# Performance work log

Measured on AMD Instinct MI355X. Metric: run time of the kernel, lower is better.

## Reference

```python
import jax, jax.numpy as jnp
import numpy as np

L, D, H, KV, HD, KVL, I, PL = 8, 2048, 8, 2, 256, 4096, 8192, 256
FULL = (4,)          # layers with full (global) attention / global RoPE
POS = 2047           # current decode position (cache write slot)
N_REP = H // KV      # GQA expansion factor


def rms(x, eps=1e-6):
    # RMSNorm without scale (v_norm); scale applied by caller where needed
    return x * jax.lax.rsqrt(jnp.mean(x * x, axis=-1, keepdims=True) + eps)


def rope(x, cos, sin):
    half = HD // 2
    rot = jnp.concatenate([-x[..., half:], x[..., :half]], axis=-1)
    return x * cos + rot * sin


def _rope_tables(theta):
    inv = 1.0 / (theta ** (np.arange(0, HD, 2, dtype=np.float32) / HD))
    ang = jnp.asarray(POS * inv, dtype=jnp.float32)
    return jnp.concatenate([jnp.cos(ang)] * 2), jnp.concatenate([jnp.sin(ang)] * 2)


def setup_inputs() -> dict:
    key = jax.random.key(0)
    ks = jax.random.split(key, 24)
    r = lambda k, s, sc=0.02: jax.random.normal(k, s, jnp.float32) * sc
    gains = lambda k, s: 1.0 + jax.random.normal(k, s, jnp.float32) * 0.02
    cos_s, sin_s = _rope_tables(10000.0)
    cos_f, sin_f = _rope_tables(1000000.0)
    um = jnp.zeros((1, 1, KVL, 1), jnp.float32).at[0, 0, POS, 0].set(1.0)
    mask = jnp.where(jnp.arange(KVL) <= POS, 0.0, -1e9).astype(jnp.float32)
    return {
        "hidden_states": r(ks[0], (1, 1, D), 1.0),
        "causal_mask": mask,
        "update_mask": um,
        "per_layer_combined": r(ks[1], (1, 1, L * PL), 1.0),
        "cos_s": cos_s, "sin_s": sin_s, "cos_f": cos_f, "sin_f": sin_f,
        "K_in": r(ks[2], (L, KV, KVL, HD)),
        "V_in": r(ks[3], (L, KV, KVL, HD)),
        "w_q": r(ks[4], (L, H * HD, D)),
        "w_k": r(ks[5], (L, KV * HD, D)),
        "w_v": r(ks[6], (L, KV * HD, D)),
        "w_o": r(ks[7], (L, D, H * HD)),
        "g_in_ln": gains(ks[8], (L, D)),
        "g_q_norm": gains(ks[9], (L, HD)),
        "g_k_norm": gains(ks[10], (L, HD)),
        "g_post_attn_ln": gains(ks[11], (L, D)),
        "g_pre_ff_ln": gains(ks[12], (L, D)),
        "g_post_ff_ln": gains(ks[13], (L, D)),
        "w_gate": r(ks[14], (L, I, D)),
        "w_up": r(ks[15], (L, I, D)),
        "w_down": r(ks[16], (L, D, I)),
        "w_plg": r(ks[17], (L, PL, D)),
        "w_plp": r(ks[18], (L, D, PL)),
        "g_post_pl_ln": gains(ks[19], (L, D)),
        "layer_scalar": jnp.ones((L,), jnp.float32),
    }


def reference(hidden_states, causal_mask, update_mask, per_layer_combined,
              cos_s, sin_s, cos_f, sin_f, K_in, V_in,
              w_q, w_k, w_v, w_o,
              g_in_ln, g_q_norm, g_k_norm, g_post_attn_ln, g_pre_ff_ln, g_post_ff_ln,
              w_gate, w_up, w_down, w_plg, w_plp, g_post_pl_ln, layer_scalar):
    um = update_mask[0, 0]          # [KVL,1] one-hot at write position
    h = hidden_states[0, 0]         # [D], batch=1/seq=1 decode
    K_outs, V_outs = [], []
    for i in range(L):
        cos, sin = (cos_f, sin_f) if i in FULL else (cos_s, sin_s)
        # --- attention block ---
        res = h
        x = rms(h) * g_in_ln[i]
        q = rms((w_q[i] @ x).reshape(H, HD)) * g_q_norm[i]
        q = rope(q, cos, sin)                                   # [H,HD]
        k = rms((w_k[i] @ x).reshape(KV, HD)) * g_k_norm[i]
        k = rope(k, cos, sin)                                   # [KV,HD]
        v = rms((w_v[i] @ x).reshape(KV, HD))                    # v_norm (no scale)
        # full-tensor masked blend = KV cache write (faithful to source)
        Ko = K_in[i] * (1.0 - um) + k[:, None, :] * um          # [KV,KVL,HD]
        Vo = V_in[i] * (1.0 - um) + v[:, None, :] * um
        K_outs.append(Ko); V_outs.append(Vo)
        Ke = jnp.repeat(Ko, N_REP, axis=0)                      # GQA expand [H,KVL,HD]
        Ve = jnp.repeat(Vo, N_REP, axis=0)
        scores = jnp.einsum('hd,hkd->hk', q, Ke) + causal_mask  # no 1/sqrt(hd) in source
        attn = jax.nn.softmax(scores, axis=-1)
        ao = jnp.einsum('hk,hkd->hd', attn, Ve).reshape(H * HD)
        ao = rms(w_o[i] @ ao) * g_post_attn_ln[i]
        h = res + ao
        # --- gated MLP ---
        res = h
        xm = rms(h) * g_pre_ff_ln[i]
        m = w_down[i] @ (jax.nn.gelu(w_gate[i] @ xm, approximate=True) * (w_up[i] @ xm))
        h = res + rms(m) * g_post_ff_ln[i]
        # --- per-layer input gating ---
        res = h
        pls = per_layer_combined[0, 0, i * PL:(i + 1) * PL]     # [PL]
        g = jax.nn.gelu(w_plg[i] @ h, approximate=True) * pls
        h = res + rms(w_plp[i] @ g) * g_post_pl_ln[i]
        h = h * layer_scalar[i]
    return (h[None, None, :], jnp.stack(K_outs), jnp.stack(V_outs))
```

## Files before the change

kernel.cpp:

```cpp
#include <hip/hip_runtime.h>

#define NL   8
#define DIM  2048
#define NH   8
#define NKV  2
#define HD   256
#define KVL  4096
#define FFI  8192
#define PLD  256
#define POS  2047
#define NCH  128
#define CP   16

__device__ __forceinline__ float dot4(float4 a, float4 b){
  return a.x*b.x + a.y*b.y + a.z*b.z + a.w*b.w;
}

__device__ __forceinline__ float waveAllSum(float v){
#pragma unroll
  for(int o=1;o<64;o<<=1) v += __shfl_xor(v,o,64);
  return v;
}

__device__ __forceinline__ float blockSum256(float v, float* red){
  int lane = threadIdx.x & 63, w = threadIdx.x >> 6;
  v = waveAllSum(v);
  __syncthreads();
  if(lane==0) red[w] = v;
  __syncthreads();
  return red[0]+red[1]+red[2]+red[3];
}

__device__ __forceinline__ float gelu_tanh(float v){
  return 0.5f*v*(1.0f + tanhf(0.7978845608028654f*(v + 0.044715f*v*v*v)));
}

__device__ __forceinline__ float4 normRope(const float* __restrict__ raw, int lane,
    const float* __restrict__ gain, const float* __restrict__ cosT,
    const float* __restrict__ sinT, bool doRope){
  float4 v4 = ((const float4*)raw)[lane];
  float ss = waveAllSum(dot4(v4,v4));
  float sc = rsqrtf(ss*(1.f/HD) + 1e-6f);
  float4 n;
  if(gain){
    float4 g4 = ((const float4*)gain)[lane];
    n.x=v4.x*sc*g4.x; n.y=v4.y*sc*g4.y; n.z=v4.z*sc*g4.z; n.w=v4.w*sc*g4.w;
  } else {
    n.x=v4.x*sc; n.y=v4.y*sc; n.z=v4.z*sc; n.w=v4.w*sc;
  }
  if(!doRope) return n;
  float4 np;
  np.x=__shfl_xor(n.x,32,64); np.y=__shfl_xor(n.y,32,64);
  np.z=__shfl_xor(n.z,32,64); np.w=__shfl_xor(n.w,32,64);
  float4 c4 = ((const float4*)cosT)[lane];
  float4 s4 = ((const float4*)sinT)[lane];
  float sg = (lane < 32) ? -1.f : 1.f;
  float4 o;
  o.x = n.x*c4.x + sg*np.x*s4.x;
  o.y = n.y*c4.y + sg*np.y*s4.y;
  o.z = n.z*c4.z + sg*np.z*s4.z;
  o.w = n.w*c4.w + sg*np.w*s4.w;
  return o;
}

__global__ __launch_bounds__(256) void qkv_k(
    const float* __restrict__ Wq, const float* __restrict__ Wk,
    const float* __restrict__ Wv,
    const float* __restrict__ hC, const float* __restrict__ u,
    const float* __restrict__ g_pl, const float* __restrict__ lsc,
    const float* __restrict__ g_in, const float* __restrict__ hidden,
    float* __restrict__ hA, float* __restrict__ qkv){
  __shared__ float xs[DIM];
  __shared__ float red[4];
  int tid = threadIdx.x;
  float hv[8];
  if(hidden){
#pragma unroll
    for(int i=0;i<8;i++) hv[i] = hidden[tid + i*256];
  } else {
    float uv[8]; float ss1 = 0.f;
#pragma unroll
    for(int i=0;i<8;i++){ uv[i] = u[tid + i*256]; ss1 += uv[i]*uv[i]; }
    ss1 = blockSum256(ss1, red);
    float r1 = rsqrtf(ss1*(1.f/DIM) + 1e-6f);
    float ls = lsc[0];
#pragma unroll
    for(int i=0;i<8;i++){
      int idx = tid + i*256;
      hv[i] = (hC[idx] + uv[i]*r1*g_pl[idx])*ls;
    }
  }
  float ss2 = 0.f;
#pragma unroll
  for(int i=0;i<8;i++) ss2 += hv[i]*hv[i];
  ss2 = blockSum256(ss2, red);
  float r2 = rsqrtf(ss2*(1.f/DIM) + 1e-6f);
#pragma unroll
  for(int i=0;i<8;i++){
    int idx = tid + i*256;
    xs[idx] = hv[i]*r2*g_in[idx];
    if(blockIdx.x==0) hA[idx] = hv[i];
  }
  __syncthreads();
  int lane = tid & 63, wv = tid >> 6;
  int r = blockIdx.x*4 + wv;
  const float* W; int row;
  if(r < 2048){ W = Wq; row = r; }
  else if(r < 2560){ W = Wk; row = r - 2048; }
  else { W = Wv; row = r - 2560; }
  const float4* Wr = (const float4*)(W + (size_t)row*DIM);
  const float4* xs4 = (const float4*)xs;
  float4 w8[8];
#pragma unroll
  for(int i=0;i<8;i++) w8[i] = Wr[i*64+lane];
  float acc = 0.f;
#pragma unroll
  for(int i=0;i<8;i++) acc += dot4(w8[i], xs4[i*64+lane]);
  acc = waveAllSum(acc);
  if(lane==0) qkv[r] = acc;
}

__global__ __launch_bounds__(256) void attn_k(
    const float* __restrict__ qkvb,
    const float* __restrict__ gq, const float* __restrict__ gk,
    const float* __restrict__ cosT, const float* __restrict__ sinT,
    float* __restrict__ Kl, float* __restrict__ Vl,
    float* __restrict__ pm, float* __restrict__ pl, float* __restrict__ po){
  int b = blockIdx.x, tid = threadIdx.x, lane = tid & 63, wv = tid >> 6;

  if(b == NKV*NCH){
    int kvv = wv >> 1, isV = wv & 1;
    const float* raw = qkvb + (isV ? 2560 : 2048) + kvv*HD;
    float4 o = normRope(raw, lane, isV ? nullptr : gk, cosT, sinT, !isV);
    float* dst = (isV ? Vl : Kl) + ((size_t)kvv*KVL + POS)*HD;
    ((float4*)dst)[lane] = o;
    return;
  }

  int kv = b & 1, c = b >> 1;
  __shared__ float q_s[4][HD];
  __shared__ float vf_s[HD];
  __shared__ float s_s[4][CP];
  __shared__ float s_w[4][CP];
  bool fresh = (c == NCH-1);

  {
    float4 o = normRope(qkvb + (kv*4 + wv)*HD, lane, gq, cosT, sinT, true);
    ((float4*)q_s[wv])[lane] = o;
  }
  float4 kf4 = {0,0,0,0};
  if(fresh){
    if(wv == 3) kf4 = normRope(qkvb + 2048 + kv*HD, lane, gk, cosT, sinT, true);
    if(wv == 1){
      float4 o = normRope(qkvb + 2560 + kv*HD, lane, nullptr, cosT, sinT, false);
      ((float4*)vf_s)[lane] = o;
    }
  }
  __syncthreads();

  float4 q4[4];
#pragma unroll
  for(int hh=0;hh<4;hh++) q4[hh] = ((const float4*)q_s[hh])[lane];
  const float4* Kp = (const float4*)(Kl + ((size_t)kv*KVL + c*CP)*HD);
#pragma unroll
  for(int j=0;j<4;j++){
    int p = wv*4 + j;
    float4 k4 = (fresh && p==CP-1) ? kf4 : Kp[(size_t)p*64 + lane];
    float d0 = dot4(k4,q4[0]), d1 = dot4(k4,q4[1]);
    float d2 = dot4(k4,q4[2]), d3 = dot4(k4,q4[3]);
    d0 = waveAllSum(d0); d1 = waveAllSum(d1);
    d2 = waveAllSum(d2); d3 = waveAllSum(d3);
    if(lane==0){ s_s[0][p]=d0; s_s[1][p]=d1; s_s[2][p]=d2; s_s[3][p]=d3; }
  }
  __syncthreads();

  if(tid < 64){
    int hh = tid >> 4, pp = tid & 15;
    float s = s_s[hh][pp];
    float m = s;
#pragma unroll
    for(int o=1;o<16;o<<=1) m = fmaxf(m, __shfl_xor(m,o,64));
    float e = __expf(s - m);
    float ls = e;
#pragma unroll
    for(int o=1;o<16;o<<=1) ls += __shfl_xor(ls,o,64);
    s_w[hh][pp] = e;
    if(pp==0){ int hg = kv*4 + hh; pm[hg*NCH + c] = m; pl[hg*NCH + c] = ls; }
  }
  __syncthreads();

  int d = tid;
  const float* Vp = Vl + ((size_t)kv*KVL + c*CP)*HD;
  float vv[CP];
#pragma unroll
  for(int p2=0;p2<CP;p2++) vv[p2] = Vp[(size_t)p2*HD + d];
  if(fresh) vv[CP-1] = vf_s[d];
  float acc[4] = {0.f,0.f,0.f,0.f};
#pragma unroll
  for(int p2=0;p2<CP;p2++){
#pragma unroll
    for(int hh=0;hh<4;hh++) acc[hh] += s_w[hh][p2]*vv[p2];
  }
#pragma unroll
  for(int hh=0;hh<4;hh++)
    po[((size_t)(kv*4+hh)*NCH + c)*HD + d] = acc[hh];
}

__global__ __launch_bounds__(256) void attn_c(const float* __restrict__ pm,
    const float* __restrict__ pl, const float* __restrict__ po, float* __restrict__ ao){
  int h = blockIdx.x, tid = threadIdx.x;
  __shared__ float sm[NCH], sl[NCH], se[NCH];
  if(tid < NCH){ sm[tid] = pm[h*NCH+tid]; sl[tid] = pl[h*NCH+tid]; }
  __syncthreads();
  float M = -1e30f;
  for(int c=0;c<NCH;c++) M = fmaxf(M, sm[c]);
  if(tid < NCH) se[tid] = __expf(sm[tid]-M);
  __syncthreads();
  float Lh = 0.f;
  for(int c=0;c<NCH;c++) Lh += sl[c]*se[c];
  float a0=0.f, a1=0.f, a2=0.f, a3=0.f;
#pragma unroll 1
  for(int c=0;c<NCH;c+=4){
    a0 += po[((size_t)h*NCH + c  )*HD + tid]*se[c];
    a1 += po[((size_t)h*NCH + c+1)*HD + tid]*se[c+1];
    a2 += po[((size_t)h*NCH + c+2)*HD + tid]*se[c+2];
    a3 += po[((size_t)h*NCH + c+3)*HD + tid]*se[c+3];
  }
  ao[h*HD + tid] = (a0+a1+a2+a3) / Lh;
}

template<int C>
__global__ __launch_bounds__(256) void gemv_k(const float* __restrict__ W,
    const float* __restrict__ x, float* __restrict__ y){
  __shared__ float xs[C];
  for(int i=threadIdx.x; i<C/4; i+=256)
    ((float4*)xs)[i] = ((const float4*)x)[i];
  __syncthreads();
  int lane = threadIdx.x & 63, wv = threadIdx.x >> 6;
  int r = blockIdx.x*4 + wv;
  const float4* Wr = (const float4*)(W + (size_t)r*C);
  const float4* xs4 = (const float4*)xs;
  float acc = 0.f;
#pragma unroll
  for(int ii=0;ii<C/2048;ii++){
    float4 w8[8];
#pragma unroll
    for(int i=0;i<8 && ii*8+i < C/256;i++) w8[i] = Wr[(ii*8+i)*64+lane];
#pragma unroll
    for(int i=0;i<8 && ii*8+i < C/256;i++) acc += dot4(w8[i], xs4[(ii*8+i)*64+lane]);
  }
  if(C < 2048){
    float4 w1 = Wr[lane];
    acc = dot4(w1, xs4[lane]);
  }
  acc = waveAllSum(acc);
  if(lane==0) y[r] = acc;
}

__global__ __launch_bounds__(256) void gateup_k(const float* __restrict__ Wg,
    const float* __restrict__ Wu, const float* __restrict__ y,
    const float* __restrict__ hA, const float* __restrict__ g_pa,
    const float* __restrict__ g_pf, float* __restrict__ hB, float* __restrict__ t){
  __shared__ float xs[DIM];
  __shared__ float red[4];
  int tid = threadIdx.x;
  float yv[8]; float ss1 = 0.f;
#pragma unroll
  for(int i=0;i<8;i++){ yv[i] = y[tid + i*256]; ss1 += yv[i]*yv[i]; }
  ss1 = blockSum256(ss1, red);
  float r1 = rsqrtf(ss1*(1.f/DIM) + 1e-6f);
  float hv[8]; float ss2 = 0.f;
#pragma unroll
  for(int i=0;i<8;i++){
    int idx = tid + i*256;
    hv[i] = hA[idx] + yv[i]*r1*g_pa[idx];
    ss2 += hv[i]*hv[i];
  }
  ss2 = blockSum256(ss2, red);
  float r2 = rsqrtf(ss2*(1.f/DIM) + 1e-6f);
#pragma unroll
  for(int i=0;i<8;i++){
    int idx = tid + i*256;
    xs[idx] = hv[i]*r2*g_pf[idx];
    if(blockIdx.x==0) hB[idx] = hv[i];
  }
  __syncthreads();
  int lane = tid & 63, wv = tid >> 6;
  int j = blockIdx.x*4 + wv;
  const float4* Gr = (const float4*)(Wg + (size_t)j*DIM);
  const float4* Ur = (const float4*)(Wu + (size_t)j*DIM);
  const float4* xs4 = (const float4*)xs;
  float4 g8[8], u8[8];
#pragma unroll
  for(int i=0;i<8;i++) g8[i] = Gr[i*64+lane];
#pragma unroll
  for(int i=0;i<8;i++) u8[i] = Ur[i*64+lane];
  float ag = 0.f, au = 0.f;
#pragma unroll
  for(int i=0;i<8;i++){
    float4 bv = xs4[i*64+lane];
    ag += dot4(g8[i], bv);
    au += dot4(u8[i], bv);
  }
  ag = waveAllSum(ag);
  au = waveAllSum(au);
  if(lane==0) t[j] = gelu_tanh(ag)*au;
}

__global__ __launch_bounds__(256) void down_k(const float* __restrict__ Wd,
    const float* __restrict__ t, float* __restrict__ mv){
  __shared__ float red[4];
  int tid = threadIdx.x, lane = tid & 63, wv = tid >> 6;
  int r = blockIdx.x;
  const float4* Wr = (const float4*)(Wd + (size_t)r*FFI) + wv*512;
  const float4* tp = (const float4*)t + wv*512;
  float4 w8[8], t8[8];
#pragma unroll
  for(int i=0;i<8;i++) w8[i] = Wr[i*64+lane];
#pragma unroll
  for(int i=0;i<8;i++) t8[i] = tp[i*64+lane];
  float acc = 0.f;
#pragma unroll
  for(int i=0;i<8;i++) acc += dot4(w8[i], t8[i]);
  acc = waveAllSum(acc);
  if(lane==0) red[wv] = acc;
  __syncthreads();
  if(tid==0) mv[r] = red[0]+red[1]+red[2]+red[3];
}

__global__ __launch_bounds__(256) void plg_k(const float* __restrict__ W,
    const float* __restrict__ mv, const float* __restrict__ hB,
    const float* __restrict__ g_ff, const float* __restrict__ pls,
    float* __restrict__ hCout, float* __restrict__ gb){
  __shared__ float xs[DIM];
  __shared__ float red[4];
  int tid = threadIdx.x;
  float mvv[8]; float ss1 = 0.f;
#pragma unroll
  for(int i=0;i<8;i++){ mvv[i] = mv[tid + i*256]; ss1 += mvv[i]*mvv[i]; }
  ss1 = blockSum256(ss1, red);
  float r1 = rsqrtf(ss1*(1.f/DIM) + 1e-6f);
#pragma unroll
  for(int i=0;i<8;i++){
    int idx = tid + i*256;
    float hc = hB[idx] + mvv[i]*r1*g_ff[idx];
    xs[idx] = hc;
    if(blockIdx.x==0) hCout[idx] = hc;
  }
  __syncthreads();
  int lane = tid & 63, wv = tid >> 6;
  int r = blockIdx.x*4 + wv;
  const float4* Wr = (const float4*)(W + (size_t)r*DIM);
  const float4* xs4 = (const float4*)xs;
  float4 w8[8];
#pragma unroll
  for(int i=0;i<8;i++) w8[i] = Wr[i*64+lane];
  float acc = 0.f;
#pragma unroll
  for(int i=0;i<8;i++) acc += dot4(w8[i], xs4[i*64+lane]);
  acc = waveAllSum(acc);
  if(lane==0) gb[r] = gelu_tanh(acc)*pls[r];
}

__global__ __launch_bounds__(256) void final_k(const float* __restrict__ u,
    const float* __restrict__ hC, const float* __restrict__ g_pl,
    const float* __restrict__ lsc, float* __restrict__ out){
  __shared__ float red[4];
  int tid = threadIdx.x;
  float uv[8]; float ss1 = 0.f;
#pragma unroll
  for(int i=0;i<8;i++){ uv[i] = u[tid + i*256]; ss1 += uv[i]*uv[i]; }
  ss1 = blockSum256(ss1, red);
  float r1 = rsqrtf(ss1*(1.f/DIM) + 1e-6f);
  float ls = lsc[0];
#pragma unroll
  for(int i=0;i<8;i++){
    int idx = tid + i*256;
    out[idx] = (hC[idx] + uv[i]*r1*g_pl[idx])*ls;
  }
}

extern "C" void kernel_launch(void* const* d_in, const int* in_sizes, int n_in,
                              void* d_out, int out_size, void* d_ws, size_t ws_size,
                              hipStream_t stream){
  const float* hidden   = (const float*)d_in[0];
  const float* plc      = (const float*)d_in[3];
  const float* cos_s    = (const float*)d_in[4];
  const float* sin_s    = (const float*)d_in[5];
  const float* cos_f    = (const float*)d_in[6];
  const float* sin_f    = (const float*)d_in[7];
  const float* K_in     = (const float*)d_in[8];
  const float* V_in     = (const float*)d_in[9];
  const float* w_q      = (const float*)d_in[10];
  const float* w_k      = (const float*)d_in[11];
  const float* w_v      = (const float*)d_in[12];
  const float* w_o      = (const float*)d_in[13];
  const float* g_in_ln  = (const float*)d_in[14];
  const float* g_q_norm = (const float*)d_in[15];
  const float* g_k_norm = (const float*)d_in[16];
  const float* g_pa_ln  = (const float*)d_in[17];
  const float* g_pf_ln  = (const float*)d_in[18];
  const float* g_ff_ln  = (const float*)d_in[19];
  const float* w_gate   = (const float*)d_in[20];
  const float* w_up     = (const float*)d_in[21];
  const float* w_down   = (const float*)d_in[22];
  const float* w_plg    = (const float*)d_in[23];
  const float* w_plp    = (const float*)d_in[24];
  const float* g_pl_ln  = (const float*)d_in[25];
  const float* l_scal   = (const float*)d_in[26];

  float* out  = (float*)d_out;
  float* outK = out + DIM;
  float* outV = outK + (size_t)NL*NKV*KVL*HD;

  float* ws   = (float*)d_ws;
  float* hA   = ws;
  float* hB   = ws + 2048;
  float* hC   = ws + 4096;
  float* qkvb = ws + 6144;
  float* y    = ws + 9216;
  float* t    = ws + 11264;
  float* mv   = ws + 19456;
  float* gb   = ws + 21504;
  float* u    = ws + 21760;
  float* pm   = ws + 23808;
  float* pl   = ws + 24832;
  float* po   = ws + 25856;
  float* ao   = ws + 288000;

  (void)hipMemcpyAsync(outK, K_in, (size_t)NL*NKV*KVL*HD*sizeof(float),
                       hipMemcpyDeviceToDevice, stream);
  (void)hipMemcpyAsync(outV, V_in, (size_t)NL*NKV*KVL*HD*sizeof(float),
                       hipMemcpyDeviceToDevice, stream);

  for(int l=0;l<NL;l++){
    const float* cosT = (l==4) ? cos_f : cos_s;
    const float* sinT = (l==4) ? sin_f : sin_s;
    float* Kl = outK + (size_t)l*NKV*KVL*HD;
    float* Vl = outV + (size_t)l*NKV*KVL*HD;

    qkv_k<<<768,256,0,stream>>>(
        w_q + (size_t)l*NH*HD*DIM, w_k + (size_t)l*NKV*HD*DIM,
        w_v + (size_t)l*NKV*HD*DIM,
        hC, u,
        (l>0) ? g_pl_ln + (size_t)(l-1)*DIM : g_pl_ln,
        (l>0) ? l_scal + (l-1) : l_scal,
        g_in_ln + (size_t)l*DIM,
        (l==0) ? hidden : nullptr,
        hA, qkvb);

    attn_k<<<NKV*NCH+1,256,0,stream>>>(qkvb, g_q_norm + l*HD, g_k_norm + l*HD,
                                       cosT, sinT, Kl, Vl, pm, pl, po);

    attn_c<<<NH,256,0,stream>>>(pm, pl, po, ao);

    gemv_k<DIM><<<512,256,0,stream>>>(w_o + (size_t)l*DIM*NH*HD, ao, y);

    gateup_k<<<FFI/4,256,0,stream>>>(w_gate + (size_t)l*FFI*DIM,
                                     w_up + (size_t)l*FFI*DIM,
                                     y, hA, g_pa_ln + (size_t)l*DIM,
                                     g_pf_ln + (size_t)l*DIM, hB, t);

    down_k<<<DIM,256,0,stream>>>(w_down + (size_t)l*DIM*FFI, t, mv);

    plg_k<<<PLD/4,256,0,stream>>>(w_plg + (size_t)l*PLD*DIM, mv, hB,
                                  g_ff_ln + (size_t)l*DIM, plc + l*PLD, hC, gb);

    gemv_k<PLD><<<512,256,0,stream>>>(w_plp + (size_t)l*DIM*PLD, gb, u);
  }

  final_k<<<1,256,0,stream>>>(u, hC, g_pl_ln + (size_t)(NL-1)*DIM,
                              l_scal + (NL-1), out);
}
```

Before: 809.2 us.

## Fuse per-layer kernels: attn-combine+Wo, gate/up+down with atomics, plg+plp

Cuts each layer from seven launches to four. The attention combine is folded into the Wo GEMV, gate/up and down projections become one kernel that accumulates down-proj partials with atomicAdd, and the per-layer gate and projection are merged into one kernel in which every block recomputes the full plg GEMV redundantly. Attention now reads K/V from the input buffers instead of the copied output, which removes the dependency on the memcpy. Chunk count is halved and chunk size doubled. The aim is to cut launch overhead and intermediate round-trips, at the cost of atomic contention, lower parallelism in several kernels, and redundant plg work.

```diff
diff --git a/kernel.cpp b/kernel.cpp
--- a/kernel.cpp
+++ b/kernel.cpp
@@ -9,8 +9,8 @@
 #define FFI  8192
 #define PLD  256
 #define POS  2047
-#define NCH  128
-#define CP   16
+#define NCH  64
+#define CP   32
 
 __device__ __forceinline__ float dot4(float4 a, float4 b){
   return a.x*b.x + a.y*b.y + a.z*b.z + a.w*b.w;
@@ -66,10 +66,10 @@
 __global__ __launch_bounds__(256) void qkv_k(
     const float* __restrict__ Wq, const float* __restrict__ Wk,
     const float* __restrict__ Wv,
-    const float* __restrict__ hC, const float* __restrict__ u,
+    const float* __restrict__ hFF, const float* __restrict__ u,
     const float* __restrict__ g_pl, const float* __restrict__ lsc,
     const float* __restrict__ g_in, const float* __restrict__ hidden,
-    float* __restrict__ hA, float* __restrict__ qkv){
+    float* __restrict__ hRes, float* __restrict__ qkv){
   __shared__ float xs[DIM];
   __shared__ float red[4];
   int tid = threadIdx.x;
@@ -87,7 +87,7 @@
 #pragma unroll
     for(int i=0;i<8;i++){
       int idx = tid + i*256;
-      hv[i] = (hC[idx] + uv[i]*r1*g_pl[idx])*ls;
+      hv[i] = (hFF[idx] + uv[i]*r1*g_pl[idx])*ls;
     }
   }
   float ss2 = 0.f;
@@ -99,7 +99,7 @@
   for(int i=0;i<8;i++){
     int idx = tid + i*256;
     xs[idx] = hv[i]*r2*g_in[idx];
-    if(blockIdx.x==0) hA[idx] = hv[i];
+    if(blockIdx.x==0) hRes[idx] = hv[i];
   }
   __syncthreads();
   int lane = tid & 63, wv = tid >> 6;
@@ -124,6 +124,7 @@
     const float* __restrict__ qkvb,
     const float* __restrict__ gq, const float* __restrict__ gk,
     const float* __restrict__ cosT, const float* __restrict__ sinT,
+    const float* __restrict__ Ki, const float* __restrict__ Vi,
     float* __restrict__ Kl, float* __restrict__ Vl,
     float* __restrict__ pm, float* __restrict__ pl, float* __restrict__ po){
   int b = blockIdx.x, tid = threadIdx.x, lane = tid & 63, wv = tid >> 6;
@@ -144,10 +145,8 @@
   __shared__ float s_w[4][CP];
   bool fresh = (c == NCH-1);
 
-  {
-    float4 o = normRope(qkvb + (kv*4 + wv)*HD, lane, gq, cosT, sinT, true);
-    ((float4*)q_s[wv])[lane] = o;
-  }
+  { float4 o = normRope(qkvb + (kv*4 + wv)*HD, lane, gq, cosT, sinT, true);
+    ((float4*)q_s[wv])[lane] = o; }
   float4 kf4 = {0,0,0,0};
   if(fresh){
     if(wv == 3) kf4 = normRope(qkvb + 2048 + kv*HD, lane, gk, cosT, sinT, true);
@@ -161,10 +160,10 @@
   float4 q4[4];
 #pragma unroll
   for(int hh=0;hh<4;hh++) q4[hh] = ((const float4*)q_s[hh])[lane];
-  const float4* Kp = (const float4*)(Kl + ((size_t)kv*KVL + c*CP)*HD);
-#pragma unroll
-  for(int j=0;j<4;j++){
-    int p = wv*4 + j;
+  const float4* Kp = (const float4*)(Ki + ((size_t)kv*KVL + c*CP)*HD);
+#pragma unroll
+  for(int j=0;j<8;j++){
+    int p = wv*8 + j;
     float4 k4 = (fresh && p==CP-1) ? kf4 : Kp[(size_t)p*64 + lane];
     float d0 = dot4(k4,q4[0]), d1 = dot4(k4,q4[1]);
     float d2 = dot4(k4,q4[2]), d3 = dot4(k4,q4[3]);
@@ -174,96 +173,95 @@
   }
   __syncthreads();
 
-  if(tid < 64){
-    int hh = tid >> 4, pp = tid & 15;
+  if(tid < 128){
+    int hh = tid >> 5, pp = tid & 31;
     float s = s_s[hh][pp];
     float m = s;
 #pragma unroll
-    for(int o=1;o<16;o<<=1) m = fmaxf(m, __shfl_xor(m,o,64));
+    for(int o=1;o<32;o<<=1) m = fmaxf(m, __shfl_xor(m,o,64));
     float e = __expf(s - m);
     float ls = e;
 #pragma unroll
-    for(int o=1;o<16;o<<=1) ls += __shfl_xor(ls,o,64);
+    for(int o=1;o<32;o<<=1) ls += __shfl_xor(ls,o,64);
     s_w[hh][pp] = e;
     if(pp==0){ int hg = kv*4 + hh; pm[hg*NCH + c] = m; pl[hg*NCH + c] = ls; }
   }
   __syncthreads();
 
   int d = tid;
-  const float* Vp = Vl + ((size_t)kv*KVL + c*CP)*HD;
-  float vv[CP];
-#pragma unroll
-  for(int p2=0;p2<CP;p2++) vv[p2] = Vp[(size_t)p2*HD + d];
-  if(fresh) vv[CP-1] = vf_s[d];
+  const float* Vp = Vi + ((size_t)kv*KVL + c*CP)*HD;
   float acc[4] = {0.f,0.f,0.f,0.f};
-#pragma unroll
+#pragma unroll 8
   for(int p2=0;p2<CP;p2++){
-#pragma unroll
-    for(int hh=0;hh<4;hh++) acc[hh] += s_w[hh][p2]*vv[p2];
+    float vv = (fresh && p2==CP-1) ? vf_s[d] : Vp[(size_t)p2*HD + d];
+#pragma unroll
+    for(int hh=0;hh<4;hh++) acc[hh] += s_w[hh][p2]*vv;
   }
 #pragma unroll
   for(int hh=0;hh<4;hh++)
     po[((size_t)(kv*4+hh)*NCH + c)*HD + d] = acc[hh];
 }
 
-__global__ __launch_bounds__(256) void attn_c(const float* __restrict__ pm,
-    const float* __restrict__ pl, const float* __restrict__ po, float* __restrict__ ao){
-  int h = blockIdx.x, tid = threadIdx.x;
-  __shared__ float sm[NCH], sl[NCH], se[NCH];
-  if(tid < NCH){ sm[tid] = pm[h*NCH+tid]; sl[tid] = pl[h*NCH+tid]; }
-  __syncthreads();
-  float M = -1e30f;
-  for(int c=0;c<NCH;c++) M = fmaxf(M, sm[c]);
-  if(tid < NCH) se[tid] = __expf(sm[tid]-M);
-  __syncthreads();
-  float Lh = 0.f;
-  for(int c=0;c<NCH;c++) Lh += sl[c]*se[c];
-  float a0=0.f, a1=0.f, a2=0.f, a3=0.f;
+__global__ __launch_bounds__(256) void wo_k(const float* __restrict__ Wo,
+    const float* __restrict__ pm, const float* __restrict__ pl,
+    const float* __restrict__ po, float* __restrict__ y, float* __restrict__ mv){
+  __shared__ float ao_s[DIM];
+  __shared__ float se_s[NH][NCH];
+  __shared__ float Li[NH];
+  int b = blockIdx.x, tid = threadIdx.x, lane = tid & 63, wv = tid >> 6;
+  if(tid < 4){
+    float4 z = {0.f,0.f,0.f,0.f};
+    ((float4*)mv)[b*4 + tid] = z;
+  }
+  {
+    int h = tid >> 5, q2 = tid & 31;
+    float m0 = pm[h*NCH + q2], m1 = pm[h*NCH + 32 + q2];
+    float l0 = pl[h*NCH + q2], l1 = pl[h*NCH + 32 + q2];
+    float m = fmaxf(m0, m1);
+#pragma unroll
+    for(int o=1;o<32;o<<=1) m = fmaxf(m, __shfl_xor(m,o,64));
+    float e0 = __expf(m0-m), e1 = __expf(m1-m);
+    se_s[h][q2] = e0; se_s[h][q2+32] = e1;
+    float lp = l0*e0 + l1*e1;
+#pragma unroll
+    for(int o=1;o<32;o<<=1) lp += __shfl_xor(lp,o,64);
+    if(q2==0) Li[h] = 1.f/lp;
+  }
+  __syncthreads();
 #pragma unroll 1
-  for(int c=0;c<NCH;c+=4){
-    a0 += po[((size_t)h*NCH + c  )*HD + tid]*se[c];
-    a1 += po[((size_t)h*NCH + c+1)*HD + tid]*se[c+1];
-    a2 += po[((size_t)h*NCH + c+2)*HD + tid]*se[c+2];
-    a3 += po[((size_t)h*NCH + c+3)*HD + tid]*se[c+3];
-  }
-  ao[h*HD + tid] = (a0+a1+a2+a3) / Lh;
-}
-
-template<int C>
-__global__ __launch_bounds__(256) void gemv_k(const float* __restrict__ W,
-    const float* __restrict__ x, float* __restrict__ y){
-  __shared__ float xs[C];
-  for(int i=threadIdx.x; i<C/4; i+=256)
-    ((float4*)xs)[i] = ((const float4*)x)[i];
-  __syncthreads();
-  int lane = threadIdx.x & 63, wv = threadIdx.x >> 6;
-  int r = blockIdx.x*4 + wv;
-  const float4* Wr = (const float4*)(W + (size_t)r*C);
-  const float4* xs4 = (const float4*)xs;
-  float acc = 0.f;
-#pragma unroll
-  for(int ii=0;ii<C/2048;ii++){
+  for(int h=0;h<NH;h++){
+    float a = 0.f;
+#pragma unroll 8
+    for(int c=0;c<NCH;c++)
+      a += po[((size_t)(h*NCH) + c)*HD + tid]*se_s[h][c];
+    ao_s[h*HD + tid] = a*Li[h];
+  }
+  __syncthreads();
+  const float4* xs4 = (const float4*)ao_s;
+#pragma unroll
+  for(int j=0;j<4;j++){
+    int r = b*16 + wv*4 + j;
+    const float4* Wr = (const float4*)(Wo + (size_t)r*DIM);
     float4 w8[8];
 #pragma unroll
-    for(int i=0;i<8 && ii*8+i < C/256;i++) w8[i] = Wr[(ii*8+i)*64+lane];
-#pragma unroll
-    for(int i=0;i<8 && ii*8+i < C/256;i++) acc += dot4(w8[i], xs4[(ii*8+i)*64+lane]);
-  }
-  if(C < 2048){
-    float4 w1 = Wr[lane];
-    acc = dot4(w1, xs4[lane]);
-  }
-  acc = waveAllSum(acc);
-  if(lane==0) y[r] = acc;
-}
-
-__global__ __launch_bounds__(256) void gateup_k(const float* __restrict__ Wg,
-    const float* __restrict__ Wu, const float* __restrict__ y,
-    const float* __restrict__ hA, const float* __restrict__ g_pa,
-    const float* __restrict__ g_pf, float* __restrict__ hB, float* __restrict__ t){
+    for(int i=0;i<8;i++) w8[i] = Wr[i*64+lane];
+    float acc = 0.f;
+#pragma unroll
+    for(int i=0;i<8;i++) acc += dot4(w8[i], xs4[i*64+lane]);
+    acc = waveAllSum(acc);
+    if(lane==0) y[r] = acc;
+  }
+}
+
+__global__ __launch_bounds__(256) void gud_k(const float* __restrict__ Wg,
+    const float* __restrict__ Wu, const float* __restrict__ Wd,
+    const float* __restrict__ y, const float* __restrict__ hRes,
+    const float* __restrict__ gpa, const float* __restrict__ gpf,
+    float* __restrict__ hMid, float* __restrict__ mv){
   __shared__ float xs[DIM];
+  __shared__ float ts[32];
   __shared__ float red[4];
-  int tid = threadIdx.x;
+  int tid = threadIdx.x, lane = tid & 63, wv = tid >> 6;
   float yv[8]; float ss1 = 0.f;
 #pragma unroll
   for(int i=0;i<8;i++){ yv[i] = y[tid + i*256]; ss1 += yv[i]*yv[i]; }
@@ -273,7 +271,7 @@
 #pragma unroll
   for(int i=0;i<8;i++){
     int idx = tid + i*256;
-    hv[i] = hA[idx] + yv[i]*r1*g_pa[idx];
+    hv[i] = hRes[idx] + yv[i]*r1*gpa[idx];
     ss2 += hv[i]*hv[i];
   }
   ss2 = blockSum256(ss2, red);
@@ -281,60 +279,64 @@
 #pragma unroll
   for(int i=0;i<8;i++){
     int idx = tid + i*256;
-    xs[idx] = hv[i]*r2*g_pf[idx];
-    if(blockIdx.x==0) hB[idx] = hv[i];
-  }
-  __syncthreads();
-  int lane = tid & 63, wv = tid >> 6;
-  int j = blockIdx.x*4 + wv;
-  const float4* Gr = (const float4*)(Wg + (size_t)j*DIM);
-  const float4* Ur = (const float4*)(Wu + (size_t)j*DIM);
+    xs[idx] = hv[i]*r2*gpf[idx];
+    if(blockIdx.x==0) hMid[idx] = hv[i];
+  }
+  __syncthreads();
   const float4* xs4 = (const float4*)xs;
-  float4 g8[8], u8[8];
-#pragma unroll
-  for(int i=0;i<8;i++) g8[i] = Gr[i*64+lane];
-#pragma unroll
-  for(int i=0;i<8;i++) u8[i] = Ur[i*64+lane];
-  float ag = 0.f, au = 0.f;
-#pragma unroll
-  for(int i=0;i<8;i++){
-    float4 bv = xs4[i*64+lane];
-    ag += dot4(g8[i], bv);
-    au += dot4(u8[i], bv);
-  }
-  ag = waveAllSum(ag);
-  au = waveAllSum(au);
-  if(lane==0) t[j] = gelu_tanh(ag)*au;
-}
-
-__global__ __launch_bounds__(256) void down_k(const float* __restrict__ Wd,
-    const float* __restrict__ t, float* __restrict__ mv){
+  int j0 = blockIdx.x*32;
+#pragma unroll 1
+  for(int jj=0;jj<8;jj++){
+    int j = j0 + wv*8 + jj;
+    const float4* Gr = (const float4*)(Wg + (size_t)j*DIM);
+    const float4* Ur = (const float4*)(Wu + (size_t)j*DIM);
+    float4 g8[8], u8[8];
+#pragma unroll
+    for(int i=0;i<8;i++) g8[i] = Gr[i*64+lane];
+#pragma unroll
+    for(int i=0;i<8;i++) u8[i] = Ur[i*64+lane];
+    float ag = 0.f, au = 0.f;
+#pragma unroll
+    for(int i=0;i<8;i++){
+      float4 bv = xs4[i*64+lane];
+      ag += dot4(g8[i], bv);
+      au += dot4(u8[i], bv);
+    }
+    ag = waveAllSum(ag);
+    au = waveAllSum(au);
+    if(lane==0) ts[wv*8+jj] = gelu_tanh(ag)*au;
+  }
+  __syncthreads();
+  const float4* ts4 = (const float4*)ts;
+  float4 t8[8];
+#pragma unroll
+  for(int i=0;i<8;i++) t8[i] = ts4[i];
+#pragma unroll 1
+  for(int it=0;it<8;it+=2){
+    int ra = it*256 + tid, rb = (it+1)*256 + tid;
+    const float4* Wa = (const float4*)(Wd + (size_t)ra*FFI + j0);
+    const float4* Wb = (const float4*)(Wd + (size_t)rb*FFI + j0);
+    float4 wa[8], wb[8];
+#pragma unroll
+    for(int i=0;i<8;i++) wa[i] = Wa[i];
+#pragma unroll
+    for(int i=0;i<8;i++) wb[i] = Wb[i];
+    float aa = 0.f, ab = 0.f;
+#pragma unroll
+    for(int i=0;i<8;i++){ aa += dot4(wa[i], t8[i]); ab += dot4(wb[i], t8[i]); }
+    atomicAdd(&mv[ra], aa);
+    atomicAdd(&mv[rb], ab);
+  }
+}
+
+__global__ __launch_bounds__(256) void plgplp_k(const float* __restrict__ Wpg,
+    const float* __restrict__ Wpp, const float* __restrict__ mv,
+    const float* __restrict__ hMid, const float* __restrict__ gff,
+    const float* __restrict__ pls, float* __restrict__ hFF, float* __restrict__ u){
+  __shared__ float hc_s[DIM];
+  __shared__ float gb_s[PLD];
   __shared__ float red[4];
   int tid = threadIdx.x, lane = tid & 63, wv = tid >> 6;
-  int r = blockIdx.x;
-  const float4* Wr = (const float4*)(Wd + (size_t)r*FFI) + wv*512;
-  const float4* tp = (const float4*)t + wv*512;
-  float4 w8[8], t8[8];
-#pragma unroll
-  for(int i=0;i<8;i++) w8[i] = Wr[i*64+lane];
-#pragma unroll
-  for(int i=0;i<8;i++) t8[i] = tp[i*64+lane];
-  float acc = 0.f;
-#pragma unroll
-  for(int i=0;i<8;i++) acc += dot4(w8[i], t8[i]);
-  acc = waveAllSum(acc);
-  if(lane==0) red[wv] = acc;
-  __syncthreads();
-  if(tid==0) mv[r] = red[0]+red[1]+red[2]+red[3];
-}
-
-__global__ __launch_bounds__(256) void plg_k(const float* __restrict__ W,
-    const float* __restrict__ mv, const float* __restrict__ hB,
-    const float* __restrict__ g_ff, const float* __restrict__ pls,
-    float* __restrict__ hCout, float* __restrict__ gb){
-  __shared__ float xs[DIM];
-  __shared__ float red[4];
-  int tid = threadIdx.x;
   float mvv[8]; float ss1 = 0.f;
 #pragma unroll
   for(int i=0;i<8;i++){ mvv[i] = mv[tid + i*256]; ss1 += mvv[i]*mvv[i]; }
@@ -343,27 +345,39 @@
 #pragma unroll
   for(int i=0;i<8;i++){
     int idx = tid + i*256;
-    float hc = hB[idx] + mvv[i]*r1*g_ff[idx];
-    xs[idx] = hc;
-    if(blockIdx.x==0) hCout[idx] = hc;
-  }
-  __syncthreads();
-  int lane = tid & 63, wv = tid >> 6;
-  int r = blockIdx.x*4 + wv;
-  const float4* Wr = (const float4*)(W + (size_t)r*DIM);
-  const float4* xs4 = (const float4*)xs;
-  float4 w8[8];
-#pragma unroll
-  for(int i=0;i<8;i++) w8[i] = Wr[i*64+lane];
-  float acc = 0.f;
-#pragma unroll
-  for(int i=0;i<8;i++) acc += dot4(w8[i], xs4[i*64+lane]);
-  acc = waveAllSum(acc);
-  if(lane==0) gb[r] = gelu_tanh(acc)*pls[r];
+    float hc = hMid[idx] + mvv[i]*r1*gff[idx];
+    hc_s[idx] = hc;
+    if(blockIdx.x==0) hFF[idx] = hc;
+  }
+  __syncthreads();
+  const float4* hc4 = (const float4*)hc_s;
+#pragma unroll 1
+  for(int rr=0;rr<64;rr++){
+    int r = wv*64 + rr;
+    const float4* Wr = (const float4*)(Wpg + (size_t)r*DIM);
+    float4 w8[8];
+#pragma unroll
+    for(int i=0;i<8;i++) w8[i] = Wr[i*64+lane];
+    float acc = 0.f;
+#pragma unroll
+    for(int i=0;i<8;i++) acc += dot4(w8[i], hc4[i*64+lane]);
+    acc = waveAllSum(acc);
+    if(lane==0) gb_s[r] = gelu_tanh(acc)*pls[r];
+  }
+  __syncthreads();
+  const float4* gb4 = (const float4*)gb_s;
+#pragma unroll
+  for(int j=0;j<8;j++){
+    int r = blockIdx.x*32 + wv*8 + j;
+    const float4* Wr = (const float4*)(Wpp + (size_t)r*PLD);
+    float acc = dot4(Wr[lane], gb4[lane]);
+    acc = waveAllSum(acc);
+    if(lane==0) u[r] = acc;
+  }
 }
 
 __global__ __launch_bounds__(256) void final_k(const float* __restrict__ u,
-    const float* __restrict__ hC, const float* __restrict__ g_pl,
+    const float* __restrict__ hFF, const float* __restrict__ g_pl,
     const float* __restrict__ lsc, float* __restrict__ out){
   __shared__ float red[4];
   int tid = threadIdx.x;
@@ -376,7 +390,7 @@
 #pragma unroll
   for(int i=0;i<8;i++){
     int idx = tid + i*256;
-    out[idx] = (hC[idx] + uv[i]*r1*g_pl[idx])*ls;
+    out[idx] = (hFF[idx] + uv[i]*r1*g_pl[idx])*ls;
   }
 }
 
@@ -414,19 +428,16 @@
   float* outV = outK + (size_t)NL*NKV*KVL*HD;
 
   float* ws   = (float*)d_ws;
-  float* hA   = ws;
-  float* hB   = ws + 2048;
-  float* hC   = ws + 4096;
+  float* hRes = ws;
+  float* hMid = ws + 2048;
+  float* hFF  = ws + 4096;
   float* qkvb = ws + 6144;
   float* y    = ws + 9216;
-  float* t    = ws + 11264;
-  float* mv   = ws + 19456;
-  float* gb   = ws + 21504;
-  float* u    = ws + 21760;
-  float* pm   = ws + 23808;
-  float* pl   = ws + 24832;
-  float* po   = ws + 25856;
-  float* ao   = ws + 288000;
+  float* mv   = ws + 11264;
+  float* u    = ws + 13312;
+  float* pm   = ws + 15360;
+  float* pl   = ws + 15872;
+  float* po   = ws + 16384;
 
   (void)hipMemcpyAsync(outK, K_in, (size_t)NL*NKV*KVL*HD*sizeof(float),
                        hipMemcpyDeviceToDevice, stream);
@@ -438,37 +449,36 @@
     const float* sinT = (l==4) ? sin_f : sin_s;
     float* Kl = outK + (size_t)l*NKV*KVL*HD;
     float* Vl = outV + (size_t)l*NKV*KVL*HD;
+    const float* Ki = K_in + (size_t)l*NKV*KVL*HD;
+    const float* Vi = V_in + (size_t)l*NKV*KVL*HD;
 
     qkv_k<<<768,256,0,stream>>>(
         w_q + (size_t)l*NH*HD*DIM, w_k + (size_t)l*NKV*HD*DIM,
         w_v + (size_t)l*NKV*HD*DIM,
-        hC, u,
+        hFF, u,
         (l>0) ? g_pl_ln + (size_t)(l-1)*DIM : g_pl_ln,
         (l>0) ? l_scal + (l-1) : l_scal,
         g_in_ln + (size_t)l*DIM,
         (l==0) ? hidden : nullptr,
-        hA, qkvb);
+        hRes, qkvb);
 
     attn_k<<<NKV*NCH+1,256,0,stream>>>(qkvb, g_q_norm + l*HD, g_k_norm + l*HD,
-                                       cosT, sinT, Kl, Vl, pm, pl, po);
-
-    attn_c<<<NH,256,0,stream>>>(pm, pl, po, ao);
-
-    gemv_k<DIM><<<512,256,0,stream>>>(w_o + (size_t)l*DIM*NH*HD, ao, y);
-
-    gateup_k<<<FFI/4,256,0,stream>>>(w_gate + (size_t)l*FFI*DIM,
-                                     w_up + (size_t)l*FFI*DIM,
-                                     y, hA, g_pa_ln + (size_t)l*DIM,
-                                     g_pf_ln + (size_t)l*DIM, hB, t);
-
-    down_k<<<DIM,256,0,stream>>>(w_down + (size_t)l*DIM*FFI, t, mv);
-
-    plg_k<<<PLD/4,256,0,stream>>>(w_plg + (size_t)l*PLD*DIM, mv, hB,
-                                  g_ff_ln + (size_t)l*DIM, plc + l*PLD, hC, gb);
-
-    gemv_k<PLD><<<512,256,0,stream>>>(w_plp + (size_t)l*DIM*PLD, gb, u);
-  }
-
-  final_k<<<1,256,0,stream>>>(u, hC, g_pl_ln + (size_t)(NL-1)*DIM,
+                                       cosT, sinT, Ki, Vi, Kl, Vl, pm, pl, po);
+
+    wo_k<<<128,256,0,stream>>>(w_o + (size_t)l*DIM*NH*HD, pm, pl, po, y, mv);
+
+    gud_k<<<256,256,0,stream>>>(w_gate + (size_t)l*FFI*DIM,
+                                w_up + (size_t)l*FFI*DIM,
+                                w_down + (size_t)l*DIM*FFI,
+                                y, hRes, g_pa_ln + (size_t)l*DIM,
+                                g_pf_ln + (size_t)l*DIM, hMid, mv);
+
+    plgplp_k<<<64,256,0,stream>>>(w_plg + (size_t)l*PLD*DIM,
+                                  w_plp + (size_t)l*DIM*PLD,
+                                  mv, hMid, g_ff_ln + (size_t)l*DIM,
+                                  plc + l*PLD, hFF, u);
+  }
+
+  final_k<<<1,256,0,stream>>>(u, hFF, g_pl_ln + (size_t)(NL-1)*DIM,
                               l_scal + (NL-1), out);
 }
```

Measured after the change: 2.354 ms. 2.91x slower.
